# Optimization experiments

Hardware: AMD Instinct MI355X
Metric: run time of the kernel (lower is better)

## Reference

```python
import jax, jax.numpy as jnp
import numpy as np


def setup_inputs() -> dict:
    key = jax.random.key(0)
    ks = jax.random.split(key, 8)
    B, Cq, Ckv, Co, T, H, W = 2, 256, 256, 256, 8, 28, 28
    s = 1.0 / np.sqrt(Cq)
    return {
        "x": jax.random.normal(ks[0], (B, Cq, T, H, W), jnp.float32),
        "context": jax.random.normal(ks[1], (B, Ckv, T, H, W), jnp.float32),
        "wq": jax.random.normal(ks[2], (Co, Cq), jnp.float32) * s,
        "bq": jnp.zeros((Co,), jnp.float32),
        "wk": jax.random.normal(ks[3], (Co, Ckv), jnp.float32) * s,
        "bk": jnp.zeros((Co,), jnp.float32),
        "wv": jax.random.normal(ks[4], (Co, Ckv), jnp.float32) * s,
        "bv": jnp.zeros((Co,), jnp.float32),
    }


def reference(x, context, wq, bq, wk, bk, wv, bv):
    B, C, T, H, W = x.shape
    N = T * H * W
    Co = wq.shape[0]
    # 1x1x1 Conv3d == per-voxel linear projection over channels
    def proj(inp, w, b):
        y = jnp.einsum('bcthw,oc->bothw', inp, w) + b[None, :, None, None, None]
        return y.reshape(B, Co, N)  # [B, Co, N]
    q = proj(x, wq, bq).transpose(0, 2, 1)        # [B, N, Co]
    k = proj(context, wk, bk)                     # [B, Co, Nc]
    v = proj(context, wv, bv).transpose(0, 2, 1)  # [B, Nc, Co]
    scale = 1.0 / jnp.sqrt(jnp.asarray(Co, x.dtype))
    attn = jax.nn.softmax(jnp.einsum('bnc,bcm->bnm', q, k) * scale, axis=-1)
    out = jnp.einsum('bnm,bmc->bnc', attn, v)     # [B, N, Co]
    out = out.transpose(0, 2, 1).reshape(B, Co, T, H, W)
    return out + x
```

## Files before the change

kernel.cpp:

```cpp
#include <hip/hip_runtime.h>
#include <hip/hip_bf16.h>
#include <math.h>

#define BB 2
#define CC 256
#define NN 6272
#define NT16 392
#define NKB32 196
#define SCL 0.09016844005f

typedef __attribute__((ext_vector_type(8))) short s8v;
typedef __attribute__((ext_vector_type(4))) float f4v;
typedef __attribute__((ext_vector_type(4))) unsigned short us4v;

__device__ inline unsigned short f2bf(float f) {
  unsigned u = __builtin_bit_cast(unsigned, f);
  u += 0x7fffu + ((u >> 16) & 1u);
  return (unsigned short)(u >> 16);
}

__device__ inline float bf2f(unsigned short h) {
  unsigned u = (unsigned)h << 16;
  return __builtin_bit_cast(float, u);
}

__global__ __launch_bounds__(256) void wcvt_kernel(
    const float* __restrict__ wq, const float* __restrict__ wk,
    const float* __restrict__ wv, unsigned short* __restrict__ Wb)
{
  int i = (blockIdx.x * 256 + threadIdx.x) * 4;
  const float* src = (i < 65536) ? wq : (i < 131072 ? wk : wv);
  int off = i & 65535;
  float4 v = *(const float4*)(src + off);
  ushort4 o;
  o.x = f2bf(v.x); o.y = f2bf(v.y); o.z = f2bf(v.z); o.w = f2bf(v.w);
  *(ushort4*)(Wb + i) = o;
}

__global__ __launch_bounds__(256) void proj_kernel(
    const float* __restrict__ x, const float* __restrict__ ctx,
    const unsigned short* __restrict__ Wb,
    const float* __restrict__ bq, const float* __restrict__ bk,
    const float* __restrict__ bv,
    unsigned short* __restrict__ Q, unsigned short* __restrict__ Kk,
    unsigned short* __restrict__ V)
{
  const int p = blockIdx.z, b = blockIdx.y;
  const int n0 = blockIdx.x * 32;
  const int tid = threadIdx.x;
  const float* in = (p == 0 ? x : ctx) + (size_t)b * CC * NN;
  const unsigned short* W = Wb + (size_t)p * 65536;
  const float* bias = (p == 0 ? bq : (p == 1 ? bk : bv));

  __shared__ __align__(16) unsigned short lds[32][264];
  for (int it = tid; it < 2048; it += 256) {
    int c  = it >> 3;
    int n4 = (it & 7) << 2;
    float4 v = *(const float4*)(in + (size_t)c * NN + n0 + n4);
    lds[n4 + 0][c] = f2bf(v.x);
    lds[n4 + 1][c] = f2bf(v.y);
    lds[n4 + 2][c] = f2bf(v.z);
    lds[n4 + 3][c] = f2bf(v.w);
  }
  __syncthreads();

  const int lane = tid & 63, l15 = lane & 15, g = lane >> 4;
  const int obase = (tid >> 6) * 64;

  f4v acc[4][2];
#pragma unroll
  for (int mt = 0; mt < 4; ++mt) {
    float4 b4 = *(const float4*)(bias + obase + mt * 16 + g * 4);
    f4v bi = {b4.x, b4.y, b4.z, b4.w};
    acc[mt][0] = bi; acc[mt][1] = bi;
  }

#pragma unroll
  for (int ks = 0; ks < 8; ++ks) {
    s8v bf0 = *(const s8v*)(&lds[l15][ks * 32 + g * 8]);
    s8v bf1 = *(const s8v*)(&lds[16 + l15][ks * 32 + g * 8]);
#pragma unroll
    for (int mt = 0; mt < 4; ++mt) {
      s8v wa = *(const s8v*)(W + (size_t)(obase + mt * 16 + l15) * CC + ks * 32 + g * 8);
      acc[mt][0] = __builtin_amdgcn_mfma_f32_16x16x32_bf16(wa, bf0, acc[mt][0], 0, 0, 0);
      acc[mt][1] = __builtin_amdgcn_mfma_f32_16x16x32_bf16(wa, bf1, acc[mt][1], 0, 0, 0);
    }
  }

  if (p == 0) {
#pragma unroll
    for (int mt = 0; mt < 4; ++mt)
#pragma unroll
      for (int qq = 0; qq < 2; ++qq)
#pragma unroll
        for (int r = 0; r < 4; ++r)
          acc[mt][qq][r] *= SCL;
  }

  if (p < 2) {
    unsigned short* dst = (p == 0 ? Q : Kk) + (size_t)b * NN * CC;
#pragma unroll
    for (int mt = 0; mt < 4; ++mt)
#pragma unroll
      for (int qq = 0; qq < 2; ++qq) {
        ushort4 pk;
        pk.x = f2bf(acc[mt][qq][0]); pk.y = f2bf(acc[mt][qq][1]);
        pk.z = f2bf(acc[mt][qq][2]); pk.w = f2bf(acc[mt][qq][3]);
        *(ushort4*)(dst + (size_t)(n0 + qq * 16 + l15) * CC + obase + mt * 16 + g * 4) = pk;
      }
  } else {
    unsigned short* dstb = V + (size_t)b * CC * NN;
#pragma unroll
    for (int mt = 0; mt < 4; ++mt)
#pragma unroll
      for (int qq = 0; qq < 2; ++qq)
#pragma unroll
        for (int r = 0; r < 4; ++r)
          dstb[(size_t)(obase + mt * 16 + g * 4 + r) * NN + n0 + qq * 16 + l15] =
              f2bf(acc[mt][qq][r]);
  }
}

__global__ __launch_bounds__(256, 4) void attn_kernel(
    const unsigned short* __restrict__ Qg,
    const unsigned short* __restrict__ Kg,
    const unsigned short* __restrict__ Vg,
    unsigned short* __restrict__ Opart,
    float* __restrict__ ml,
    int split, int kb_base, int kb_rem)
{
  const int s     = blockIdx.x % split;
  const int stile = blockIdx.x / split;
  const int b     = stile / 98;
  const int qsup  = stile % 98;
  const int tid   = threadIdx.x;
  const int w     = tid >> 6;
  const int lane  = tid & 63;
  const int l15 = lane & 15, g = lane >> 4;
  const int qt16  = qsup * 4 + w;
  const int q0    = qt16 * 16;
  const int wid16 = b * NT16 + qt16;

  const int start = s * kb_base + (s < kb_rem ? s : kb_rem);
  const int cnt   = kb_base + (s < kb_rem ? 1 : 0);

  const unsigned short* Qb = Qg + (size_t)b * NN * CC;
  const unsigned short* Kb = Kg + (size_t)b * NN * CC;
  const unsigned short* Vb = Vg + (size_t)b * CC * NN;

  __shared__ __align__(16) unsigned short K_lds[2][32 * 256];
  __shared__ __align__(16) unsigned short V_lds[2][256 * 32];
  __shared__ __align__(16) unsigned short P_lds[4][16][36];

  s8v qf[8];
#pragma unroll
  for (int ks = 0; ks < 8; ++ks)
    qf[ks] = *(const s8v*)(Qb + (size_t)(q0 + l15) * CC + ks * 32 + g * 8);

  f4v ot[16];
  const f4v fz = {0.f, 0.f, 0.f, 0.f};
#pragma unroll
  for (int mt = 0; mt < 16; ++mt) ot[mt] = fz;

  float lsum = 0.f;

  auto stage = [&](int buf, int kb32) {
    const int kb = kb32 * 32;
#pragma unroll
    for (int i = 0; i < 8; ++i) {
      int chunk = w * 512 + i * 64 + lane;
      if (chunk < 1024) {
        int r = chunk >> 5, cc = chunk & 31;
        const unsigned short* gp =
            Kb + (size_t)(kb + r) * CC + ((cc ^ (r & 15)) << 3);
        __builtin_amdgcn_global_load_lds(
            (const __attribute__((address_space(1))) unsigned int*)gp,
            (__attribute__((address_space(3))) unsigned int*)(&K_lds[buf][chunk * 8]),
            16, 0, 0);
      } else {
        int vc = chunk - 1024;
        int ch = vc >> 2, cc = vc & 3;
        const unsigned short* gp =
            Vb + (size_t)ch * NN + kb + ((cc ^ ((ch >> 1) & 3)) << 3);
        __builtin_amdgcn_global_load_lds(
            (const __attribute__((address_space(1))) unsigned int*)gp,
            (__attribute__((address_space(3))) unsigned int*)(&V_lds[buf][vc * 8]),
            16, 0, 0);
      }
    }
  };

  stage(0, start);
  int cur = 0;

  for (int ib = 0; ib < cnt; ++ib) {
    __syncthreads();
    if (ib + 1 < cnt) stage(cur ^ 1, start + ib + 1);

    const unsigned short* Kl = &K_lds[cur][0];
    const unsigned short* Vl = &V_lds[cur][0];

    f4v st[2];
    st[0] = fz; st[1] = fz;
#pragma unroll
    for (int ks = 0; ks < 8; ++ks) {
      const int co = ((ks * 4 + g) ^ l15) << 3;
#pragma unroll
      for (int kt = 0; kt < 2; ++kt) {
        s8v ka = *(const s8v*)(Kl + (kt * 16 + l15) * 256 + co);
        st[kt] = __builtin_amdgcn_mfma_f32_16x16x32_bf16(ka, qf[ks], st[kt], 0, 0, 0);
      }
    }

#pragma unroll
    for (int kt = 0; kt < 2; ++kt) {
      float p0 = __builtin_amdgcn_exp2f(st[kt][0]);
      float p1 = __builtin_amdgcn_exp2f(st[kt][1]);
      float p2 = __builtin_amdgcn_exp2f(st[kt][2]);
      float p3 = __builtin_amdgcn_exp2f(st[kt][3]);
      lsum += (p0 + p1) + (p2 + p3);
      ushort4 pk;
      pk.x = f2bf(p0); pk.y = f2bf(p1); pk.z = f2bf(p2); pk.w = f2bf(p3);
      *(ushort4*)(&P_lds[w][l15][kt * 16 + 4 * g]) = pk;
    }

    s8v pb = *(const s8v*)(&P_lds[w][l15][g * 8]);
    const int vo = (g ^ ((l15 >> 1) & 3)) << 3;
#pragma unroll
    for (int mt = 0; mt < 16; ++mt) {
      s8v va = *(const s8v*)(Vl + (mt * 16 + l15) * 32 + vo);
      ot[mt] = __builtin_amdgcn_mfma_f32_16x16x32_bf16(va, pb, ot[mt], 0, 0, 0);
    }

    cur ^= 1;
  }

  lsum += __shfl_xor(lsum, 16);
  lsum += __shfl_xor(lsum, 32);

  unsigned short* Ob = Opart + (size_t)(wid16 * split + s) * 4096;
#pragma unroll
  for (int mt = 0; mt < 16; ++mt) {
    us4v o4;
    o4.x = f2bf(ot[mt][0]); o4.y = f2bf(ot[mt][1]);
    o4.z = f2bf(ot[mt][2]); o4.w = f2bf(ot[mt][3]);
    __builtin_nontemporal_store(o4, (us4v*)(Ob + mt * 256 + lane * 4));
  }

  if (lane < 16)
    ml[(size_t)(wid16 * split + s) * 16 + lane] = lsum;
}

__global__ __launch_bounds__(256) void merge_kernel(
    const unsigned short* __restrict__ Opart,
    const float* __restrict__ ml,
    const float* __restrict__ x,
    float* __restrict__ out,
    int split)
{
  const int wid32 = blockIdx.x;
  const int b  = wid32 / (NT16 / 2);
  const int pi = wid32 % (NT16 / 2);
  const int n0 = pi * 32;
  const int tid = threadIdx.x;
  const int w = tid >> 6;
  const int lane = tid & 63;
  const int l15 = lane & 15, g = lane >> 4;

  __shared__ float lds_o[256][33];

#pragma unroll
  for (int t = 0; t < 2; ++t) {
    const int wid16 = b * NT16 + pi * 2 + t;
    float L = 0.f;
#pragma unroll
    for (int s = 0; s < 8; ++s)
      if (s < split)
        L += ml[(size_t)(wid16 * split + s) * 16 + l15];
    const float invL = 1.f / L;

#pragma unroll
    for (int j = 0; j < 4; ++j) {
      int mt = j * 4 + w;
      float a0 = 0.f, a1 = 0.f, a2 = 0.f, a3 = 0.f;
#pragma unroll
      for (int s = 0; s < 8; ++s)
        if (s < split) {
          const us4v* Op4 = (const us4v*)(Opart + (size_t)(wid16 * split + s) * 4096);
          us4v o4 = __builtin_nontemporal_load(Op4 + mt * 64 + lane);
          a0 += bf2f(o4.x); a1 += bf2f(o4.y);
          a2 += bf2f(o4.z); a3 += bf2f(o4.w);
        }
      int c = mt * 16 + g * 4;
      int nl = t * 16 + l15;
      lds_o[c + 0][nl] = a0 * invL;
      lds_o[c + 1][nl] = a1 * invL;
      lds_o[c + 2][nl] = a2 * invL;
      lds_o[c + 3][nl] = a3 * invL;
    }
  }
  __syncthreads();

  const size_t base = (size_t)b * CC * NN + n0;
  const int n = tid & 31;
  const int c0 = tid >> 5;
#pragma unroll
  for (int cg = 0; cg < 32; ++cg) {
    int c = cg * 8 + c0;
    size_t idx = base + (size_t)c * NN + n;
    out[idx] = lds_o[c][n] + x[idx];
  }
}

extern "C" void kernel_launch(void* const* d_in, const int* in_sizes, int n_in,
                              void* d_out, int out_size, void* d_ws, size_t ws_size,
                              hipStream_t stream) {
  const float* x   = (const float*)d_in[0];
  const float* ctx = (const float*)d_in[1];
  const float* wq  = (const float*)d_in[2];
  const float* bq  = (const float*)d_in[3];
  const float* wk  = (const float*)d_in[4];
  const float* bk  = (const float*)d_in[5];
  const float* wv  = (const float*)d_in[6];
  const float* bv  = (const float*)d_in[7];
  float* out = (float*)d_out;

  const size_t sz = (size_t)BB * NN * CC;
  unsigned short* Wb = (unsigned short*)d_ws;
  unsigned short* Q  = Wb + 3 * 65536;
  unsigned short* K  = Q + sz;
  unsigned short* V  = K + sz;
  const size_t fixedB = 3 * 65536 * 2 + 3 * sz * 2;

  int split = 1;
  const int cands[3] = {5, 2, 1};
  for (int i = 0; i < 3; ++i) {
    size_t need = fixedB + (size_t)cands[i] * (BB * NT16) *
                  (4096 * sizeof(unsigned short) + 16 * sizeof(float));
    if (ws_size >= need) { split = cands[i]; break; }
  }
  unsigned short* Opart = (unsigned short*)((char*)d_ws + fixedB);
  float* ml = (float*)(Opart + (size_t)split * (BB * NT16) * 4096);
  const int kb_base = NKB32 / split, kb_rem = NKB32 % split;

  wcvt_kernel<<<dim3(192), dim3(256), 0, stream>>>(wq, wk, wv, Wb);
  proj_kernel<<<dim3(NN / 32, BB, 3), dim3(256), 0, stream>>>(
      x, ctx, Wb, bq, bk, bv, Q, K, V);
  attn_kernel<<<dim3(196 * split), dim3(256), 0, stream>>>(
      Q, K, V, Opart, ml, split, kb_base, kb_rem);
  merge_kernel<<<dim3(BB * NT16 / 2), dim3(256), 0, stream>>>(
      Opart, ml, x, out, split);
}
```

Before: 258.3 us.

## Fuse K/V projections per block and single-buffer attention K/V staging

Result: slower. 312.9 us (+21.2%).

```diff
diff --git a/kernel.cpp b/kernel.cpp
--- a/kernel.cpp
+++ b/kernel.cpp
@@ -49,8 +49,6 @@
   const int n0 = blockIdx.x * 32;
   const int tid = threadIdx.x;
   const float* in = (p == 0 ? x : ctx) + (size_t)b * CC * NN;
-  const unsigned short* W = Wb + (size_t)p * 65536;
-  const float* bias = (p == 0 ? bq : (p == 1 ? bk : bv));
 
   __shared__ __align__(16) unsigned short lds[32][264];
   for (int it = tid; it < 2048; it += 256) {
@@ -67,57 +65,79 @@
   const int lane = tid & 63, l15 = lane & 15, g = lane >> 4;
   const int obase = (tid >> 6) * 64;
 
-  f4v acc[4][2];
-#pragma unroll
-  for (int mt = 0; mt < 4; ++mt) {
-    float4 b4 = *(const float4*)(bias + obase + mt * 16 + g * 4);
-    f4v bi = {b4.x, b4.y, b4.z, b4.w};
-    acc[mt][0] = bi; acc[mt][1] = bi;
-  }
-
-#pragma unroll
-  for (int ks = 0; ks < 8; ++ks) {
-    s8v bf0 = *(const s8v*)(&lds[l15][ks * 32 + g * 8]);
-    s8v bf1 = *(const s8v*)(&lds[16 + l15][ks * 32 + g * 8]);
+  if (p == 0) {
+    const unsigned short* W = Wb;
+    f4v acc[4][2];
 #pragma unroll
     for (int mt = 0; mt < 4; ++mt) {
-      s8v wa = *(const s8v*)(W + (size_t)(obase + mt * 16 + l15) * CC + ks * 32 + g * 8);
-      acc[mt][0] = __builtin_amdgcn_mfma_f32_16x16x32_bf16(wa, bf0, acc[mt][0], 0, 0, 0);
-      acc[mt][1] = __builtin_amdgcn_mfma_f32_16x16x32_bf16(wa, bf1, acc[mt][1], 0, 0, 0);
-    }
-  }
-
-  if (p == 0) {
-#pragma unroll
-    for (int mt = 0; mt < 4; ++mt)
-#pragma unroll
-      for (int qq = 0; qq < 2; ++qq)
-#pragma unroll
-        for (int r = 0; r < 4; ++r)
-          acc[mt][qq][r] *= SCL;
-  }
-
-  if (p < 2) {
-    unsigned short* dst = (p == 0 ? Q : Kk) + (size_t)b * NN * CC;
+      float4 b4 = *(const float4*)(bq + obase + mt * 16 + g * 4);
+      f4v bi = {b4.x, b4.y, b4.z, b4.w};
+      acc[mt][0] = bi; acc[mt][1] = bi;
+    }
+#pragma unroll
+    for (int ks = 0; ks < 8; ++ks) {
+      s8v bf0 = *(const s8v*)(&lds[l15][ks * 32 + g * 8]);
+      s8v bf1 = *(const s8v*)(&lds[16 + l15][ks * 32 + g * 8]);
+#pragma unroll
+      for (int mt = 0; mt < 4; ++mt) {
+        s8v wa = *(const s8v*)(W + (size_t)(obase + mt * 16 + l15) * CC + ks * 32 + g * 8);
+        acc[mt][0] = __builtin_amdgcn_mfma_f32_16x16x32_bf16(wa, bf0, acc[mt][0], 0, 0, 0);
+        acc[mt][1] = __builtin_amdgcn_mfma_f32_16x16x32_bf16(wa, bf1, acc[mt][1], 0, 0, 0);
+      }
+    }
+    unsigned short* dst = Q + (size_t)b * NN * CC;
 #pragma unroll
     for (int mt = 0; mt < 4; ++mt)
 #pragma unroll
       for (int qq = 0; qq < 2; ++qq) {
         ushort4 pk;
-        pk.x = f2bf(acc[mt][qq][0]); pk.y = f2bf(acc[mt][qq][1]);
-        pk.z = f2bf(acc[mt][qq][2]); pk.w = f2bf(acc[mt][qq][3]);
+        pk.x = f2bf(acc[mt][qq][0] * SCL); pk.y = f2bf(acc[mt][qq][1] * SCL);
+        pk.z = f2bf(acc[mt][qq][2] * SCL); pk.w = f2bf(acc[mt][qq][3] * SCL);
         *(ushort4*)(dst + (size_t)(n0 + qq * 16 + l15) * CC + obase + mt * 16 + g * 4) = pk;
       }
   } else {
-    unsigned short* dstb = V + (size_t)b * CC * NN;
+    const unsigned short* WK = Wb + 65536;
+    const unsigned short* WV = Wb + 131072;
+    f4v accK[4][2], accV[4][2];
+#pragma unroll
+    for (int mt = 0; mt < 4; ++mt) {
+      float4 k4 = *(const float4*)(bk + obase + mt * 16 + g * 4);
+      float4 v4 = *(const float4*)(bv + obase + mt * 16 + g * 4);
+      f4v ki = {k4.x, k4.y, k4.z, k4.w};
+      f4v vi = {v4.x, v4.y, v4.z, v4.w};
+      accK[mt][0] = ki; accK[mt][1] = ki;
+      accV[mt][0] = vi; accV[mt][1] = vi;
+    }
+#pragma unroll
+    for (int ks = 0; ks < 8; ++ks) {
+      s8v bf0 = *(const s8v*)(&lds[l15][ks * 32 + g * 8]);
+      s8v bf1 = *(const s8v*)(&lds[16 + l15][ks * 32 + g * 8]);
+#pragma unroll
+      for (int mt = 0; mt < 4; ++mt) {
+        size_t wo = (size_t)(obase + mt * 16 + l15) * CC + ks * 32 + g * 8;
+        s8v wk8 = *(const s8v*)(WK + wo);
+        s8v wv8 = *(const s8v*)(WV + wo);
+        accK[mt][0] = __builtin_amdgcn_mfma_f32_16x16x32_bf16(wk8, bf0, accK[mt][0], 0, 0, 0);
+        accK[mt][1] = __builtin_amdgcn_mfma_f32_16x16x32_bf16(wk8, bf1, accK[mt][1], 0, 0, 0);
+        accV[mt][0] = __builtin_amdgcn_mfma_f32_16x16x32_bf16(wv8, bf0, accV[mt][0], 0, 0, 0);
+        accV[mt][1] = __builtin_amdgcn_mfma_f32_16x16x32_bf16(wv8, bf1, accV[mt][1], 0, 0, 0);
+      }
+    }
+    unsigned short* dstK = Kk + (size_t)b * NN * CC;
+    unsigned short* dstV = V + (size_t)b * CC * NN;
 #pragma unroll
     for (int mt = 0; mt < 4; ++mt)
 #pragma unroll
-      for (int qq = 0; qq < 2; ++qq)
+      for (int qq = 0; qq < 2; ++qq) {
+        ushort4 pk;
+        pk.x = f2bf(accK[mt][qq][0]); pk.y = f2bf(accK[mt][qq][1]);
+        pk.z = f2bf(accK[mt][qq][2]); pk.w = f2bf(accK[mt][qq][3]);
+        *(ushort4*)(dstK + (size_t)(n0 + qq * 16 + l15) * CC + obase + mt * 16 + g * 4) = pk;
 #pragma unroll
         for (int r = 0; r < 4; ++r)
-          dstb[(size_t)(obase + mt * 16 + g * 4 + r) * NN + n0 + qq * 16 + l15] =
-              f2bf(acc[mt][qq][r]);
+          dstV[(size_t)(obase + mt * 16 + g * 4 + r) * NN + n0 + qq * 16 + l15] =
+              f2bf(accV[mt][qq][r]);
+      }
   }
 }
 
@@ -148,8 +168,7 @@
   const unsigned short* Kb = Kg + (size_t)b * NN * CC;
   const unsigned short* Vb = Vg + (size_t)b * CC * NN;
 
-  __shared__ __align__(16) unsigned short K_lds[2][32 * 256];
-  __shared__ __align__(16) unsigned short V_lds[2][256 * 32];
+  __shared__ __align__(16) unsigned short KV[32 * 256 + 256 * 32];
   __shared__ __align__(16) unsigned short P_lds[4][16][36];
 
   s8v qf[8];
@@ -164,41 +183,44 @@
 
   float lsum = 0.f;
 
-  auto stage = [&](int buf, int kb32) {
-    const int kb = kb32 * 32;
+  unsigned off[8];
+  const unsigned short* gbase;
+  int step;
+  int ldsbase;
+  if (w < 2) {
+    gbase = Kb; step = 32 * CC;
+    ldsbase = w * 4096;
 #pragma unroll
     for (int i = 0; i < 8; ++i) {
       int chunk = w * 512 + i * 64 + lane;
-      if (chunk < 1024) {
-        int r = chunk >> 5, cc = chunk & 31;
-        const unsigned short* gp =
-            Kb + (size_t)(kb + r) * CC + ((cc ^ (r & 15)) << 3);
-        __builtin_amdgcn_global_load_lds(
-            (const __attribute__((address_space(1))) unsigned int*)gp,
-            (__attribute__((address_space(3))) unsigned int*)(&K_lds[buf][chunk * 8]),
-            16, 0, 0);
-      } else {
-        int vc = chunk - 1024;
-        int ch = vc >> 2, cc = vc & 3;
-        const unsigned short* gp =
-            Vb + (size_t)ch * NN + kb + ((cc ^ ((ch >> 1) & 3)) << 3);
-        __builtin_amdgcn_global_load_lds(
-            (const __attribute__((address_space(1))) unsigned int*)gp,
-            (__attribute__((address_space(3))) unsigned int*)(&V_lds[buf][vc * 8]),
-            16, 0, 0);
-      }
-    }
-  };
-
-  stage(0, start);
-  int cur = 0;
+      int r = chunk >> 5, cc = chunk & 31;
+      off[i] = (unsigned)((start * 32 + r) * CC + ((cc ^ (r & 15)) << 3));
+    }
+  } else {
+    gbase = Vb; step = 32;
+    ldsbase = 8192 + (w - 2) * 4096;
+#pragma unroll
+    for (int i = 0; i < 8; ++i) {
+      int vc = (w - 2) * 512 + i * 64 + lane;
+      int ch = vc >> 2, cc = vc & 3;
+      off[i] = (unsigned)(ch * NN + start * 32 + ((cc ^ ((ch >> 1) & 3)) << 3));
+    }
+  }
+
+  const unsigned short* Kl = KV;
+  const unsigned short* Vl = KV + 8192;
 
   for (int ib = 0; ib < cnt; ++ib) {
+    if (ib) __syncthreads();
+#pragma unroll
+    for (int i = 0; i < 8; ++i) {
+      __builtin_amdgcn_global_load_lds(
+          (const __attribute__((address_space(1))) unsigned int*)(gbase + off[i]),
+          (__attribute__((address_space(3))) unsigned int*)(&KV[ldsbase + i * 512]),
+          16, 0, 0);
+      off[i] += step;
+    }
     __syncthreads();
-    if (ib + 1 < cnt) stage(cur ^ 1, start + ib + 1);
-
-    const unsigned short* Kl = &K_lds[cur][0];
-    const unsigned short* Vl = &V_lds[cur][0];
 
     f4v st[2];
     st[0] = fz; st[1] = fz;
@@ -231,8 +253,6 @@
       s8v va = *(const s8v*)(Vl + (mt * 16 + l15) * 32 + vo);
       ot[mt] = __builtin_amdgcn_mfma_f32_16x16x32_bf16(va, pb, ot[mt], 0, 0, 0);
     }
-
-    cur ^= 1;
   }
 
   lsum += __shfl_xor(lsum, 16);
@@ -344,7 +364,7 @@
   const int kb_base = NKB32 / split, kb_rem = NKB32 % split;
 
   wcvt_kernel<<<dim3(192), dim3(256), 0, stream>>>(wq, wk, wv, Wb);
-  proj_kernel<<<dim3(NN / 32, BB, 3), dim3(256), 0, stream>>>(
+  proj_kernel<<<dim3(NN / 32, BB, 2), dim3(256), 0, stream>>>(
       x, ctx, Wb, bq, bk, bv, Q, K, V);
   attn_kernel<<<dim3(196 * split), dim3(256), 0, stream>>>(
       Q, K, V, Opart, ml, split, kb_base, kb_rem);
```
